# Performance work log

Hardware: AMD Instinct MI355X
Metric: run time of the kernel (lower is better)

Reference implementation:

```python
import jax, jax.numpy as jnp
import numpy as np

N, CH = 65536, 256
B, K, CTX = 8, 256, 768
H, D = 8, 64
NPB = N // B  # points per batch (scene)


def setup_inputs() -> dict:
    key = jax.random.key(0)
    ks = jax.random.split(key, 8)
    xF = jax.random.normal(ks[0], (N, CH), dtype=jnp.float32)
    context = jax.random.normal(ks[1], (B, K, CTX), dtype=jnp.float32)
    # decomposition_permutations: a random partition of the N sparse points into B groups
    perm = jax.random.permutation(ks[2], N).reshape(B, NPB).astype(jnp.int32)
    Wq = jax.random.normal(ks[3], (CH, H * D), dtype=jnp.float32) * 0.02
    Wk = jax.random.normal(ks[4], (CTX, H * D), dtype=jnp.float32) * 0.02
    Wv = jax.random.normal(ks[5], (CTX, H * D), dtype=jnp.float32) * 0.02
    Wout = jax.random.normal(ks[6], (H * D, CH), dtype=jnp.float32) * 0.02
    b_out = jnp.zeros((CH,), dtype=jnp.float32)
    return {"xF": xF, "context": context, "perm": perm,
            "Wq": Wq, "Wk": Wk, "Wv": Wv, "Wout": Wout, "b_out": b_out}


def reference(xF, context, perm, Wq, Wk, Wv, Wout, b_out):
    scale = D ** -0.5
    q = (xF @ Wq).reshape(N, H, D)                     # to_q (1x1 conv == linear)
    k = (context @ Wk).reshape(B, K, H, D)             # to_k
    v = (context @ Wv).reshape(B, K, H, D)             # to_v
    qg = q[perm]                                        # gather: [B, NPB, H, D]
    attn = jax.nn.softmax(scale * jnp.einsum('bqhd,bkhd->bhqk', qg, k), axis=-1)
    o = jnp.einsum('bhqk,bkhd->bqhd', attn, v).reshape(B * NPB, H * D)
    # inverse-permutation scatter back to sparse-tensor order: ft[inv_perm]
    ft = jnp.zeros((N, H * D), o.dtype).at[perm.reshape(-1)].set(o)
    out = ft @ Wout + b_out                             # to_out
    return out + xF                                     # residual
```

## Files before the change

kernel.cpp:

```cpp
#include <hip/hip_runtime.h>

typedef unsigned short u16;
typedef __attribute__((ext_vector_type(8))) short bf16x8;
typedef __attribute__((ext_vector_type(4))) float f32x4;
typedef __attribute__((ext_vector_type(4))) int i32x4;
typedef __attribute__((ext_vector_type(2))) int i32x2;

#define N_PTS   65536
#define CH_DIM  256
#define BATCH   8
#define KTOK    256
#define CTX_DIM 768
#define NHEAD   8
#define HD      64
#define HDIM    512
#define NPB     8192

__device__ __forceinline__ u16 f2bf(float f) {
    union { float f; unsigned u; } v; v.f = f;
    unsigned r = v.u + 0x7fffu + ((v.u >> 16) & 1u);
    return (u16)(r >> 16);
}
__device__ __forceinline__ unsigned cvtpk(float lo, float hi) {
    unsigned r;
    asm("v_cvt_pk_bf16_f32 %0, %1, %2" : "=v"(r) : "v"(lo), "v"(hi));
    return r;
}
__device__ __forceinline__ float exp2_hw(float x) {
    float r;
    asm("v_exp_f32 %0, %1" : "=v"(r) : "v"(x));
    return r;
}
__device__ __forceinline__ float max3f(float a, float b, float c) {
    float r;
    asm("v_max3_f32 %0, %1, %2, %3" : "=v"(r) : "v"(a), "v"(b), "v"(c));
    return r;
}

__device__ __forceinline__ void gll16(const void* g, void* l) {
    __builtin_amdgcn_global_load_lds(
        (const __attribute__((address_space(1))) void*)g,
        (__attribute__((address_space(3))) void*)l, 16, 0, 0);
}

__global__ void convk(const float* __restrict__ src, u16* __restrict__ dst, int n8) {
    int i = blockIdx.x * blockDim.x + threadIdx.x;
    int st = gridDim.x * blockDim.x;
    for (; i < n8; i += st) {
        const float* p = src + (size_t)i * 8;
        f32x4 a = *(const f32x4*)p;
        f32x4 b = *(const f32x4*)(p + 4);
        i32x4 o;
        o[0] = (int)cvtpk(a[0], a[1]);
        o[1] = (int)cvtpk(a[2], a[3]);
        o[2] = (int)cvtpk(b[0], b[1]);
        o[3] = (int)cvtpk(b[2], b[3]);
        *(i32x4*)&dst[(size_t)i * 8] = o;
    }
}

__global__ void tconvk(const float* __restrict__ W, u16* __restrict__ WT, int R, int C) {
    int i = blockIdx.x * blockDim.x + threadIdx.x;
    if (i >= R * C) return;
    int c = i / R, r = i - c * R;
    WT[(size_t)c * R + r] = f2bf(W[(size_t)r * C + c]);
}

template <bool OUT_F32, bool VT_OUT>
__global__ __launch_bounds__(256, 3) void gemm_bt(
    const u16* __restrict__ A, const u16* __restrict__ BT, void* __restrict__ Cv,
    int M, int N, int K,
    const float* __restrict__ bias, const float* __restrict__ resid, float oscale)
{
    __shared__ __align__(16) u16 As[2][128 * 32];
    __shared__ __align__(16) u16 Bs[2][128 * 32];

    const int tid  = threadIdx.x;
    const int lane = tid & 63;
    const int w    = tid >> 6;
    const int wm   = w & 1;
    const int wn   = w >> 1;

    const int nwg = gridDim.x * gridDim.y;
    const int wg  = blockIdx.y * gridDim.x + blockIdx.x;
    const int swz = (wg & 7) * (nwg >> 3) + (wg >> 3);
    const int n0  = (swz % gridDim.x) * 128;
    const int m0  = (swz / gridDim.x) * 128;

    const int l15  = lane & 15;
    const int quad = lane >> 4;

    f32x4 acc[4][4];
#pragma unroll
    for (int i = 0; i < 4; i++)
#pragma unroll
        for (int j = 0; j < 4; j++) { acc[i][j][0]=0.f; acc[i][j][1]=0.f; acc[i][j][2]=0.f; acc[i][j][3]=0.f; }

    const int sr = tid >> 2;
    const int sc = (tid & 3) * 8;
    const u16* Abase = A  + (size_t)(m0 + sr) * K + sc;
    const u16* Bbase = BT + (size_t)(n0 + sr) * K + sc;
    const size_t rowStep = (size_t)64 * K;
    const int d8 = tid * 8;

    gll16(Abase,           &As[0][d8]);
    gll16(Abase + rowStep, &As[0][d8 + 2048]);
    gll16(Bbase,           &Bs[0][d8]);
    gll16(Bbase + rowStep, &Bs[0][d8 + 2048]);
    asm volatile("s_waitcnt vmcnt(0)" ::: "memory");
    __builtin_amdgcn_s_barrier();
    __builtin_amdgcn_sched_barrier(0);

    const int ntile = K >> 5;
    int cur = 0;
    for (int t = 0; t < ntile; ++t) {
        if (t + 1 < ntile) {
            const u16* An = Abase + ((t + 1) << 5);
            const u16* Bn = Bbase + ((t + 1) << 5);
            const int nxt = cur ^ 1;
            gll16(An,           &As[nxt][d8]);
            gll16(An + rowStep, &As[nxt][d8 + 2048]);
            gll16(Bn,           &Bs[nxt][d8]);
            gll16(Bn + rowStep, &Bs[nxt][d8 + 2048]);
        }
        bf16x8 af[4], bfr[4];
#pragma unroll
        for (int rt = 0; rt < 4; rt++)
            af[rt] = *(const bf16x8*)&As[cur][(wm * 64 + rt * 16 + l15) * 32 + quad * 8];
#pragma unroll
        for (int nt = 0; nt < 4; nt++)
            bfr[nt] = *(const bf16x8*)&Bs[cur][(wn * 64 + nt * 16 + l15) * 32 + quad * 8];
#pragma unroll
        for (int rt = 0; rt < 4; rt++)
#pragma unroll
            for (int nt = 0; nt < 4; nt++)
                acc[rt][nt] = __builtin_amdgcn_mfma_f32_16x16x32_bf16(af[rt], bfr[nt], acc[rt][nt], 0, 0, 0);
        asm volatile("s_waitcnt vmcnt(0)" ::: "memory");
        __builtin_amdgcn_sched_barrier(0);
        __builtin_amdgcn_s_barrier();
        __builtin_amdgcn_sched_barrier(0);
        cur ^= 1;
    }

    if (VT_OUT) {
        u16* CT = (u16*)Cv;
#pragma unroll
        for (int nt = 0; nt < 4; nt++) {
            int col = n0 + wn * 64 + nt * 16 + l15;
            int hh = col >> 6, dd = col & 63;
#pragma unroll
            for (int rt = 0; rt < 4; rt++) {
                int row = m0 + wm * 64 + rt * 16 + quad * 4;
                int bb = row >> 8, jb = row & 255;
                int jp = (jb & 0xE0) | ((jb & 0x0C) << 1) | ((jb & 0x10) >> 2);
                union { unsigned u[2]; i32x2 q; } pk;
                pk.u[0] = cvtpk(acc[rt][nt][0], acc[rt][nt][1]);
                pk.u[1] = cvtpk(acc[rt][nt][2], acc[rt][nt][3]);
                *(i32x2*)&CT[(((size_t)(bb * 8 + hh)) * 64 + dd) * 256 + jp] = pk.q;
            }
        }
    } else {
#pragma unroll
        for (int nt = 0; nt < 4; nt++) {
            int col = n0 + wn * 64 + nt * 16 + l15;
            float bv = bias ? bias[col] : 0.0f;
#pragma unroll
            for (int rt = 0; rt < 4; rt++) {
#pragma unroll
                for (int r = 0; r < 4; r++) {
                    int row = m0 + wm * 64 + rt * 16 + quad * 4 + r;
                    float v = acc[rt][nt][r] + bv;
                    if (resid) v += resid[(size_t)row * N + col];
                    if (OUT_F32) ((float*)Cv)[(size_t)row * N + col] = v;
                    else         ((u16*)Cv)[(size_t)row * N + col]   = f2bf(v * oscale);
                }
            }
        }
    }
}

__global__ __launch_bounds__(256, 4) void gemm_kv(
    const u16* __restrict__ A, const u16* __restrict__ BT,
    u16* __restrict__ kd, u16* __restrict__ vtd)
{
    __shared__ __align__(16) u16 As[2][64 * 32];
    __shared__ __align__(16) u16 Bs[2][64 * 32];
    const int K = CTX_DIM;

    const int tid  = threadIdx.x;
    const int lane = tid & 63;
    const int w    = tid >> 6;
    const int wm   = w & 1;
    const int wn   = w >> 1;

    const int nwg = gridDim.x * gridDim.y;
    const int wg  = blockIdx.y * gridDim.x + blockIdx.x;
    const int swz = (wg & 7) * (nwg >> 3) + (wg >> 3);
    const int n0  = (swz % gridDim.x) * 64;
    const int m0  = (swz / gridDim.x) * 64;

    const int l15  = lane & 15;
    const int quad = lane >> 4;

    f32x4 acc[2][2];
#pragma unroll
    for (int i = 0; i < 2; i++)
#pragma unroll
        for (int j = 0; j < 2; j++) { acc[i][j][0]=0.f; acc[i][j][1]=0.f; acc[i][j][2]=0.f; acc[i][j][3]=0.f; }

    const int sr = tid >> 2;
    const int sc = (tid & 3) * 8;
    const u16* Abase = A  + (size_t)(m0 + sr) * K + sc;
    const u16* Bbase = BT + (size_t)(n0 + sr) * K + sc;
    const int d8 = tid * 8;

    gll16(Abase, &As[0][d8]);
    gll16(Bbase, &Bs[0][d8]);
    asm volatile("s_waitcnt vmcnt(0)" ::: "memory");
    __builtin_amdgcn_s_barrier();
    __builtin_amdgcn_sched_barrier(0);

    const int ntile = K >> 5;
    int cur = 0;
    for (int t = 0; t < ntile; ++t) {
        if (t + 1 < ntile) {
            const int nxt = cur ^ 1;
            gll16(Abase + ((t + 1) << 5), &As[nxt][d8]);
            gll16(Bbase + ((t + 1) << 5), &Bs[nxt][d8]);
        }
        bf16x8 af[2], bfr[2];
#pragma unroll
        for (int rt = 0; rt < 2; rt++)
            af[rt] = *(const bf16x8*)&As[cur][(wm * 32 + rt * 16 + l15) * 32 + quad * 8];
#pragma unroll
        for (int nt = 0; nt < 2; nt++)
            bfr[nt] = *(const bf16x8*)&Bs[cur][(wn * 32 + nt * 16 + l15) * 32 + quad * 8];
#pragma unroll
        for (int rt = 0; rt < 2; rt++)
#pragma unroll
            for (int nt = 0; nt < 2; nt++)
                acc[rt][nt] = __builtin_amdgcn_mfma_f32_16x16x32_bf16(af[rt], bfr[nt], acc[rt][nt], 0, 0, 0);
        asm volatile("s_waitcnt vmcnt(0)" ::: "memory");
        __builtin_amdgcn_sched_barrier(0);
        __builtin_amdgcn_s_barrier();
        __builtin_amdgcn_sched_barrier(0);
        cur ^= 1;
    }

    if (n0 < 512) {
#pragma unroll
        for (int nt = 0; nt < 2; nt++) {
            int col = n0 + wn * 32 + nt * 16 + l15;
#pragma unroll
            for (int rt = 0; rt < 2; rt++) {
#pragma unroll
                for (int r = 0; r < 4; r++) {
                    int row = m0 + wm * 32 + rt * 16 + quad * 4 + r;
                    kd[(size_t)row * HDIM + col] = f2bf(acc[rt][nt][r]);
                }
            }
        }
    } else {
#pragma unroll
        for (int nt = 0; nt < 2; nt++) {
            int col = (n0 - 512) + wn * 32 + nt * 16 + l15;
            int hh = col >> 6, dd = col & 63;
#pragma unroll
            for (int rt = 0; rt < 2; rt++) {
                int row = m0 + wm * 32 + rt * 16 + quad * 4;
                int bb = row >> 8, jb = row & 255;
                int jp = (jb & 0xE0) | ((jb & 0x0C) << 1) | ((jb & 0x10) >> 2);
                union { unsigned u[2]; i32x2 q; } pk;
                pk.u[0] = cvtpk(acc[rt][nt][0], acc[rt][nt][1]);
                pk.u[1] = cvtpk(acc[rt][nt][2], acc[rt][nt][3]);
                *(i32x2*)&vtd[(((size_t)(bb * 8 + hh)) * 64 + dd) * 256 + jp] = pk.q;
            }
        }
    }
}

#define KS2 72
#define VS2 264
__global__ __launch_bounds__(256, 4) void attn_mfma(
    const u16* qbuf, const u16* __restrict__ kbuf,
    const u16* __restrict__ vbufT, const int* __restrict__ perm,
    u16* ft)
{
    __shared__ __align__(16) u16 smem[18432];
    u16* Ks = smem;
    u16* Vt = smem;

    const int tid   = threadIdx.x;
    const int lane  = tid & 63;
    const int w     = tid >> 6;
    const int chunk = blockIdx.x;
    const int bh    = blockIdx.y;
    const int b     = bh >> 3;
    const int h     = bh & 7;
    const int l15   = lane & 15;
    const int quad  = lane >> 4;

    const int prow = perm[b * NPB + chunk * 64 + w * 16 + l15];
    const u16* qrow = qbuf + (size_t)prow * HDIM + h * HD;
    bf16x8 qf0 = *(const bf16x8*)&qrow[quad * 8];
    bf16x8 qf1 = *(const bf16x8*)&qrow[32 + quad * 8];

    {
        const int j8 = tid >> 3;
        const int c  = (tid & 7) * 8;
#pragma unroll
        for (int pass = 0; pass < 8; pass++) {
            int jj = j8 + pass * 32;
            i32x4 val = *(const i32x4*)&kbuf[((size_t)(b * KTOK + jj)) * HDIM + h * HD + c];
            *(i32x4*)&Ks[jj * KS2 + c] = val;
        }
    }
    __syncthreads();

    f32x4 sc[16];
#pragma unroll
    for (int nt = 0; nt < 16; nt++) { sc[nt][0]=0.f; sc[nt][1]=0.f; sc[nt][2]=0.f; sc[nt][3]=0.f; }
#pragma unroll
    for (int nt = 0; nt < 16; nt++) {
        bf16x8 kf = *(const bf16x8*)&Ks[(nt * 16 + l15) * KS2 + quad * 8];
        sc[nt] = __builtin_amdgcn_mfma_f32_16x16x32_bf16(kf, qf0, sc[nt], 0, 0, 0);
    }
#pragma unroll
    for (int nt = 0; nt < 16; nt++) {
        bf16x8 kf = *(const bf16x8*)&Ks[(nt * 16 + l15) * KS2 + 32 + quad * 8];
        sc[nt] = __builtin_amdgcn_mfma_f32_16x16x32_bf16(kf, qf1, sc[nt], 0, 0, 0);
    }

    i32x4 vreg[8];
    const u16* vslice = vbufT + ((size_t)(b * NHEAD + h)) * HD * KTOK;
    const int vrow = tid >> 2;
    const int vc0  = (tid & 3) * 8;
#pragma unroll
    for (int pass = 0; pass < 8; pass++)
        vreg[pass] = *(const i32x4*)&vslice[(size_t)vrow * KTOK + vc0 + pass * 32];

    float m = -1e30f;
#pragma unroll
    for (int nt = 0; nt < 16; nt++) {
        f32x4 v = sc[nt];
        m = max3f(m, max3f(v[0], v[1], v[2]), v[3]);
    }
    m = fmaxf(m, __shfl_xor(m, 16));
    m = fmaxf(m, __shfl_xor(m, 32));
    float s0 = 0.f, s1 = 0.f, s2 = 0.f, s3 = 0.f;
#pragma unroll
    for (int nt = 0; nt < 16; nt++) {
        float e0 = exp2_hw(sc[nt][0] - m);
        float e1 = exp2_hw(sc[nt][1] - m);
        float e2 = exp2_hw(sc[nt][2] - m);
        float e3 = exp2_hw(sc[nt][3] - m);
        sc[nt][0] = e0; sc[nt][1] = e1; sc[nt][2] = e2; sc[nt][3] = e3;
        s0 += e0; s1 += e1; s2 += e2; s3 += e3;
    }
    float s = (s0 + s1) + (s2 + s3);
    s += __shfl_xor(s, 16);
    s += __shfl_xor(s, 32);
    float inv = 1.0f / s;

    unsigned up[16][2];
#pragma unroll
    for (int nt = 0; nt < 16; nt++) {
        up[nt][0] = cvtpk(sc[nt][0], sc[nt][1]);
        up[nt][1] = cvtpk(sc[nt][2], sc[nt][3]);
    }

    __syncthreads();

#pragma unroll
    for (int pass = 0; pass < 8; pass++)
        *(i32x4*)&Vt[vrow * VS2 + vc0 + pass * 32] = vreg[pass];
    __syncthreads();

    f32x4 o[4];
#pragma unroll
    for (int n = 0; n < 4; n++) { o[n][0]=0.f; o[n][1]=0.f; o[n][2]=0.f; o[n][3]=0.f; }

#pragma unroll
    for (int ks = 0; ks < 8; ks++) {
        union { unsigned u[4]; bf16x8 v; } pb;
        pb.u[0] = up[2 * ks][0];
        pb.u[1] = up[2 * ks][1];
        pb.u[2] = up[2 * ks + 1][0];
        pb.u[3] = up[2 * ks + 1][1];
#pragma unroll
        for (int nt = 0; nt < 4; nt++) {
            bf16x8 bv = *(const bf16x8*)&Vt[(nt * 16 + l15) * VS2 + ks * 32 + quad * 8];
            o[nt] = __builtin_amdgcn_mfma_f32_16x16x32_bf16(pb.v, bv, o[nt], 0, 0, 0);
        }
    }

#pragma unroll
    for (int r = 0; r < 4; r++) {
        float invq = __shfl(inv,  quad * 4 + r);
        int   po   = __shfl(prow, quad * 4 + r);
        u16* frow = ft + (size_t)po * HDIM + h * HD;
        unsigned pa = cvtpk(o[0][r] * invq, o[1][r] * invq);
        unsigned pb = cvtpk(o[2][r] * invq, o[3][r] * invq);
        frow[l15]      = (u16)pa;
        frow[16 + l15] = (u16)(pa >> 16);
        frow[32 + l15] = (u16)pb;
        frow[48 + l15] = (u16)(pb >> 16);
    }
}

extern "C" void kernel_launch(void* const* d_in, const int* in_sizes, int n_in,
                              void* d_out, int out_size, void* d_ws, size_t ws_size,
                              hipStream_t stream) {
    const float* xF      = (const float*)d_in[0];
    const float* context = (const float*)d_in[1];
    const int*   perm    = (const int*)d_in[2];
    const float* Wq      = (const float*)d_in[3];
    const float* Wk      = (const float*)d_in[4];
    const float* Wv      = (const float*)d_in[5];
    const float* Wout    = (const float*)d_in[6];
    const float* b_out   = (const float*)d_in[7];
    float*       out     = (float*)d_out;

    const size_t WS_NEED = 71303168ULL;
    if (ws_size < WS_NEED) {
        hipMemsetAsync(d_out, 0, (size_t)out_size * sizeof(float), stream);
        return;
    }
    char* ws    = (char*)d_ws;
    u16* kbuf   = (u16*)(ws + 0);
    u16* vbufT  = (u16*)(ws + 2097152);
    u16* qbuf   = (u16*)(ws + 4194304);
    u16* ft     = qbuf;
    u16* WoutT  = (u16*)(ws + 2097152);

    char* ob    = (char*)d_out;
    u16* xb     = (u16*)(ob + 0);
    u16* cb     = (u16*)(ob + 33554432);
    u16* WkvT   = (u16*)(ob + 36700160);
    u16* WqT    = (u16*)(ob + 38273024);

    convk<<<2048, 256, 0, stream>>>(xF, xb, N_PTS * CH_DIM / 8);
    convk<<<768, 256, 0, stream>>>(context, cb, BATCH * KTOK * CTX_DIM / 8);
    tconvk<<<(CH_DIM * HDIM + 255) / 256, 256, 0, stream>>>(Wq, WqT, CH_DIM, HDIM);
    tconvk<<<(CTX_DIM * HDIM + 255) / 256, 256, 0, stream>>>(Wk, WkvT, CTX_DIM, HDIM);
    tconvk<<<(CTX_DIM * HDIM + 255) / 256, 256, 0, stream>>>(Wv, WkvT + 512 * 768, CTX_DIM, HDIM);

    gemm_bt<false, false><<<dim3(HDIM / 128, N_PTS / 128), 256, 0, stream>>>(
        xb, WqT, qbuf, N_PTS, HDIM, CH_DIM, nullptr, nullptr, 0.1803368801f);
    gemm_kv<<<dim3(16, 32), 256, 0, stream>>>(cb, WkvT, kbuf, vbufT);

    attn_mfma<<<dim3(NPB / 64, BATCH * NHEAD), 256, 0, stream>>>(
        qbuf, kbuf, vbufT, perm, ft);

    tconvk<<<(HDIM * CH_DIM + 255) / 256, 256, 0, stream>>>(Wout, WoutT, HDIM, CH_DIM);
    gemm_bt<true, false><<<dim3(CH_DIM / 128, N_PTS / 128), 256, 0, stream>>>(
        ft, WoutT, out, N_PTS, CH_DIM, HDIM, b_out, xF, 1.0f);
}
```

Baseline: 301.2 us.

## Triple-buffer GEMM K-tiles with partial vmcnt waits and merge weight transposes

Both GEMM kernels move from double to triple buffering in LDS. Three K-tiles are prefetched and the loop waits with partial vmcnt counts instead of draining all loads every iteration. K becomes a compile-time template parameter so the loop fully unrolls. The three weight transpose launches are merged into one kernel to save launch overhead. The cost is more LDS per block, which could lower occupancy for the 128x128 GEMM.

```diff
diff --git a/kernel.cpp b/kernel.cpp
--- a/kernel.cpp
+++ b/kernel.cpp
@@ -62,18 +62,34 @@
 __global__ void tconvk(const float* __restrict__ W, u16* __restrict__ WT, int R, int C) {
     int i = blockIdx.x * blockDim.x + threadIdx.x;
     if (i >= R * C) return;
-    int c = i / R, r = i - c * R;
-    WT[(size_t)c * R + r] = f2bf(W[(size_t)r * C + c]);
-}
-
-template <bool OUT_F32, bool VT_OUT>
+    WT[i] = f2bf(W[(size_t)(i % R) * C + i / R]);
+}
+
+__global__ void tconv3k(const float* __restrict__ Wq, const float* __restrict__ Wk,
+                        const float* __restrict__ Wv,
+                        u16* __restrict__ WqT, u16* __restrict__ WkvT) {
+    int i = blockIdx.x * blockDim.x + threadIdx.x;
+    if (i < 131072) {
+        WqT[i] = f2bf(Wq[(size_t)(i % 256) * 512 + i / 256]);
+    } else if (i < 524288) {
+        int j = i - 131072;
+        WkvT[j] = f2bf(Wk[(size_t)(j % 768) * 512 + j / 768]);
+    } else if (i < 917504) {
+        int j = i - 524288;
+        WkvT[393216 + j] = f2bf(Wv[(size_t)(j % 768) * 512 + j / 768]);
+    }
+}
+
+template <int KC, bool OUT_F32, bool VT_OUT>
 __global__ __launch_bounds__(256, 3) void gemm_bt(
     const u16* __restrict__ A, const u16* __restrict__ BT, void* __restrict__ Cv,
-    int M, int N, int K,
+    int M, int N,
     const float* __restrict__ bias, const float* __restrict__ resid, float oscale)
 {
-    __shared__ __align__(16) u16 As[2][128 * 32];
-    __shared__ __align__(16) u16 Bs[2][128 * 32];
+    constexpr int NT = KC / 32;
+    static_assert(NT >= 3, "need >=3 K-tiles");
+    __shared__ __align__(16) u16 As[3][128 * 32];
+    __shared__ __align__(16) u16 Bs[3][128 * 32];
 
     const int tid  = threadIdx.x;
     const int lane = tid & 63;
@@ -98,48 +114,50 @@
 
     const int sr = tid >> 2;
     const int sc = (tid & 3) * 8;
-    const u16* Abase = A  + (size_t)(m0 + sr) * K + sc;
-    const u16* Bbase = BT + (size_t)(n0 + sr) * K + sc;
-    const size_t rowStep = (size_t)64 * K;
+    const u16* Abase = A  + (size_t)(m0 + sr) * KC + sc;
+    const u16* Bbase = BT + (size_t)(n0 + sr) * KC + sc;
+    const size_t rowStep = (size_t)64 * KC;
     const int d8 = tid * 8;
 
-    gll16(Abase,           &As[0][d8]);
-    gll16(Abase + rowStep, &As[0][d8 + 2048]);
-    gll16(Bbase,           &Bs[0][d8]);
-    gll16(Bbase + rowStep, &Bs[0][d8 + 2048]);
-    asm volatile("s_waitcnt vmcnt(0)" ::: "memory");
-    __builtin_amdgcn_s_barrier();
-    __builtin_amdgcn_sched_barrier(0);
-
-    const int ntile = K >> 5;
-    int cur = 0;
-    for (int t = 0; t < ntile; ++t) {
-        if (t + 1 < ntile) {
-            const u16* An = Abase + ((t + 1) << 5);
-            const u16* Bn = Bbase + ((t + 1) << 5);
-            const int nxt = cur ^ 1;
-            gll16(An,           &As[nxt][d8]);
-            gll16(An + rowStep, &As[nxt][d8 + 2048]);
-            gll16(Bn,           &Bs[nxt][d8]);
-            gll16(Bn + rowStep, &Bs[nxt][d8 + 2048]);
-        }
+    auto stage = [&](int t, int buf) {
+        const u16* Ap = Abase + t * 32;
+        const u16* Bp = Bbase + t * 32;
+        gll16(Ap,           &As[buf][d8]);
+        gll16(Ap + rowStep, &As[buf][d8 + 2048]);
+        gll16(Bp,           &Bs[buf][d8]);
+        gll16(Bp + rowStep, &Bs[buf][d8 + 2048]);
+    };
+
+    stage(0, 0); stage(1, 1); stage(2, 2);
+
+#pragma unroll
+    for (int t = 0; t < NT; ++t) {
+        const int rem = NT - 1 - t;
+        if (rem >= 2)      asm volatile("s_waitcnt vmcnt(8)" ::: "memory");
+        else if (rem == 1) asm volatile("s_waitcnt vmcnt(4)" ::: "memory");
+        else               asm volatile("s_waitcnt vmcnt(0)" ::: "memory");
+        __builtin_amdgcn_sched_barrier(0);
+        __builtin_amdgcn_s_barrier();
+        __builtin_amdgcn_sched_barrier(0);
+
+        const int buf = t % 3;
         bf16x8 af[4], bfr[4];
 #pragma unroll
         for (int rt = 0; rt < 4; rt++)
-            af[rt] = *(const bf16x8*)&As[cur][(wm * 64 + rt * 16 + l15) * 32 + quad * 8];
+            af[rt] = *(const bf16x8*)&As[buf][(wm * 64 + rt * 16 + l15) * 32 + quad * 8];
 #pragma unroll
         for (int nt = 0; nt < 4; nt++)
-            bfr[nt] = *(const bf16x8*)&Bs[cur][(wn * 64 + nt * 16 + l15) * 32 + quad * 8];
+            bfr[nt] = *(const bf16x8*)&Bs[buf][(wn * 64 + nt * 16 + l15) * 32 + quad * 8];
 #pragma unroll
         for (int rt = 0; rt < 4; rt++)
 #pragma unroll
             for (int nt = 0; nt < 4; nt++)
                 acc[rt][nt] = __builtin_amdgcn_mfma_f32_16x16x32_bf16(af[rt], bfr[nt], acc[rt][nt], 0, 0, 0);
-        asm volatile("s_waitcnt vmcnt(0)" ::: "memory");
+
         __builtin_amdgcn_sched_barrier(0);
         __builtin_amdgcn_s_barrier();
         __builtin_amdgcn_sched_barrier(0);
-        cur ^= 1;
+        if (t + 3 < NT) stage(t + 3, buf);
     }
 
     if (VT_OUT) {
@@ -183,9 +201,10 @@
     const u16* __restrict__ A, const u16* __restrict__ BT,
     u16* __restrict__ kd, u16* __restrict__ vtd)
 {
-    __shared__ __align__(16) u16 As[2][64 * 32];
-    __shared__ __align__(16) u16 Bs[2][64 * 32];
-    const int K = CTX_DIM;
+    constexpr int KC = CTX_DIM;
+    constexpr int NT = KC / 32;
+    __shared__ __align__(16) u16 As[3][64 * 32];
+    __shared__ __align__(16) u16 Bs[3][64 * 32];
 
     const int tid  = threadIdx.x;
     const int lane = tid & 63;
@@ -210,41 +229,45 @@
 
     const int sr = tid >> 2;
     const int sc = (tid & 3) * 8;
-    const u16* Abase = A  + (size_t)(m0 + sr) * K + sc;
-    const u16* Bbase = BT + (size_t)(n0 + sr) * K + sc;
+    const u16* Abase = A  + (size_t)(m0 + sr) * KC + sc;
+    const u16* Bbase = BT + (size_t)(n0 + sr) * KC + sc;
     const int d8 = tid * 8;
 
-    gll16(Abase, &As[0][d8]);
-    gll16(Bbase, &Bs[0][d8]);
-    asm volatile("s_waitcnt vmcnt(0)" ::: "memory");
-    __builtin_amdgcn_s_barrier();
-    __builtin_amdgcn_sched_barrier(0);
-
-    const int ntile = K >> 5;
-    int cur = 0;
-    for (int t = 0; t < ntile; ++t) {
-        if (t + 1 < ntile) {
-            const int nxt = cur ^ 1;
-            gll16(Abase + ((t + 1) << 5), &As[nxt][d8]);
-            gll16(Bbase + ((t + 1) << 5), &Bs[nxt][d8]);
-        }
+    auto stage = [&](int t, int buf) {
+        gll16(Abase + t * 32, &As[buf][d8]);
+        gll16(Bbase + t * 32, &Bs[buf][d8]);
+    };
+
+    stage(0, 0); stage(1, 1); stage(2, 2);
+
+#pragma unroll
+    for (int t = 0; t < NT; ++t) {
+        const int rem = NT - 1 - t;
+        if (rem >= 2)      asm volatile("s_waitcnt vmcnt(4)" ::: "memory");
+        else if (rem == 1) asm volatile("s_waitcnt vmcnt(2)" ::: "memory");
+        else               asm volatile("s_waitcnt vmcnt(0)" ::: "memory");
+        __builtin_amdgcn_sched_barrier(0);
+        __builtin_amdgcn_s_barrier();
+        __builtin_amdgcn_sched_barrier(0);
+
+        const int buf = t % 3;
         bf16x8 af[2], bfr[2];
 #pragma unroll
         for (int rt = 0; rt < 2; rt++)
-            af[rt] = *(const bf16x8*)&As[cur][(wm * 32 + rt * 16 + l15) * 32 + quad * 8];
+            af[rt] = *(const bf16x8*)&As[buf][(wm * 32 + rt * 16 + l15) * 32 + quad * 8];
 #pragma unroll
         for (int nt = 0; nt < 2; nt++)
-            bfr[nt] = *(const bf16x8*)&Bs[cur][(wn * 32 + nt * 16 + l15) * 32 + quad * 8];
+            bfr[nt] = *(const bf16x8*)&Bs[buf][(wn * 32 + nt * 16 + l15) * 32 + quad * 8];
 #pragma unroll
         for (int rt = 0; rt < 2; rt++)
 #pragma unroll
             for (int nt = 0; nt < 2; nt++)
                 acc[rt][nt] = __builtin_amdgcn_mfma_f32_16x16x32_bf16(af[rt], bfr[nt], acc[rt][nt], 0, 0, 0);
-        asm volatile("s_waitcnt vmcnt(0)" ::: "memory");
+
         __builtin_amdgcn_sched_barrier(0);
         __builtin_amdgcn_s_barrier();
         __builtin_amdgcn_sched_barrier(0);
-        cur ^= 1;
+        if (t + 3 < NT) stage(t + 3, buf);
     }
 
     if (n0 < 512) {
@@ -441,18 +464,16 @@
 
     convk<<<2048, 256, 0, stream>>>(xF, xb, N_PTS * CH_DIM / 8);
     convk<<<768, 256, 0, stream>>>(context, cb, BATCH * KTOK * CTX_DIM / 8);
-    tconvk<<<(CH_DIM * HDIM + 255) / 256, 256, 0, stream>>>(Wq, WqT, CH_DIM, HDIM);
-    tconvk<<<(CTX_DIM * HDIM + 255) / 256, 256, 0, stream>>>(Wk, WkvT, CTX_DIM, HDIM);
-    tconvk<<<(CTX_DIM * HDIM + 255) / 256, 256, 0, stream>>>(Wv, WkvT + 512 * 768, CTX_DIM, HDIM);
-
-    gemm_bt<false, false><<<dim3(HDIM / 128, N_PTS / 128), 256, 0, stream>>>(
-        xb, WqT, qbuf, N_PTS, HDIM, CH_DIM, nullptr, nullptr, 0.1803368801f);
+    tconv3k<<<3584, 256, 0, stream>>>(Wq, Wk, Wv, WqT, WkvT);
+
+    gemm_bt<CH_DIM, false, false><<<dim3(HDIM / 128, N_PTS / 128), 256, 0, stream>>>(
+        xb, WqT, qbuf, N_PTS, HDIM, nullptr, nullptr, 0.1803368801f);
     gemm_kv<<<dim3(16, 32), 256, 0, stream>>>(cb, WkvT, kbuf, vbufT);
 
     attn_mfma<<<dim3(NPB / 64, BATCH * NHEAD), 256, 0, stream>>>(
         qbuf, kbuf, vbufT, perm, ft);
 
     tconvk<<<(HDIM * CH_DIM + 255) / 256, 256, 0, stream>>>(Wout, WoutT, HDIM, CH_DIM);
-    gemm_bt<true, false><<<dim3(CH_DIM / 128, N_PTS / 128), 256, 0, stream>>>(
-        ft, WoutT, out, N_PTS, CH_DIM, HDIM, b_out, xF, 1.0f);
-}
+    gemm_bt<HDIM, true, false><<<dim3(CH_DIM / 128, N_PTS / 128), 256, 0, stream>>>(
+        ft, WoutT, out, N_PTS, CH_DIM, b_out, xF, 1.0f);
+}
```

Measured after the change: 310.3 us. 3.0% more time.
